# Kernel optimization log

Measured on AMD Instinct MI355X. Metric: run time of the kernel, lower is better.

The kernel has to match this reference:

```python
import jax, jax.numpy as jnp
import numpy as np

N = 50000
H = 8          # heads
C = 10         # out channels per head
F_IN = 128
NEG_SLOPE = 0.2


def _glorot(key, shape, fan_in):
    return jax.random.normal(key, shape, dtype=jnp.float32) / np.sqrt(fan_in)


def setup_inputs() -> dict:
    key = jax.random.key(0)
    ks = jax.random.split(key, 16)
    x = jax.random.normal(ks[0], (N, F_IN), dtype=jnp.float32)
    edge_index = jax.random.randint(ks[1], (2, 1600000), 0, N, dtype=jnp.int64)
    inp = {"x": x, "edge_index": edge_index}
    dims = [F_IN, H * C, H * C]  # input dim of each of the 3 layers
    k = 2
    for i, din in enumerate(dims):
        inp[f"Wl{i}"] = _glorot(ks[k + 0], (din, H * C), din)
        inp[f"Wr{i}"] = _glorot(ks[k + 1], (din, H * C), din)
        inp[f"att{i}"] = _glorot(ks[k + 2], (H, C), C)
        inp[f"b{i}"] = jnp.zeros((H * C,), dtype=jnp.float32)
        k += 3
    return inp


def gatv2_layer(x, Wl, Wr, att, b, src, dst):
    # GATv2Conv (PyG defaults): separate lin_l/lin_r, e = att . leaky_relu(xl_j + xr_i),
    # segment softmax over incoming edges, scatter-add of alpha * xl_j, concat heads + bias.
    n = x.shape[0]
    xl = (x @ Wl).reshape(n, H, C)
    xr = (x @ Wr).reshape(n, H, C)
    e = jax.nn.leaky_relu(xl[src] + xr[dst], NEG_SLOPE)      # [E, H, C]
    score = jnp.einsum('ehc,hc->eh', e, att)                 # [E, H]
    smax = jax.ops.segment_max(score, dst, num_segments=n)   # [N, H]
    ex = jnp.exp(score - smax[dst])
    denom = jax.ops.segment_sum(ex, dst, num_segments=n)
    alpha = ex / (denom[dst] + 1e-16)                        # [E, H]
    out = jax.ops.segment_sum(alpha[:, :, None] * xl[src], dst, num_segments=n)
    return out.reshape(n, H * C) + b


def reference(x, edge_index, Wl0, Wr0, att0, b0, Wl1, Wr1, att1, b1, Wl2, Wr2, att2, b2):
    n = x.shape[0]
    # add_self_loops=True (PyG default)
    loop = jnp.arange(n, dtype=edge_index.dtype)
    src = jnp.concatenate([edge_index[0], loop])
    dst = jnp.concatenate([edge_index[1], loop])
    params = [(Wl0, Wr0, att0, b0), (Wl1, Wr1, att1, b1), (Wl2, Wr2, att2, b2)]
    for Wl, Wr, att, b in params:
        x = jax.nn.elu(gatv2_layer(x, Wl, Wr, att, b, src, dst))
    return x
```

## Files before the change

### kernel.cpp

```cpp
#include <hip/hip_runtime.h>
#include <hip/hip_bf16.h>
#include <hip/hip_fp16.h>

#define N_NODES 50000
#define HEADS 8
#define CHANS 10
#define HC 80
#define PHL 80
#define F_IN 128
#define E_EDGES 1600000
#define E_TOT (E_EDGES + N_NODES)
#define NEG_SLOPE 0.2f
#define NBUCK 3125
#define NCHUNK 128
#define CHUNK ((E_TOT + NCHUNK - 1) / NCHUNK)
#define GEMM_TILES ((N_NODES + 127) / 128)
#define NSLICE 4
#define SLICE_W 12500
#define XS_STRIDE 40
#define WS_STRIDE 40

typedef _Float16 f16x8 __attribute__((ext_vector_type(8)));
typedef float f32x4 __attribute__((ext_vector_type(4)));

#if __has_builtin(__builtin_amdgcn_fdot2) && __has_builtin(__builtin_elementwise_max)
#define USE_PK 1
typedef _Float16 h2 __attribute__((ext_vector_type(2)));
#else
#define USE_PK 0
#endif

__device__ inline void load_edge(const void* ei, int is64, int e, int& src, int& dst) {
    if (e < E_EDGES) {
        if (is64) {
            src = ((const int*)ei)[2 * e];
            dst = ((const int*)ei)[2 * (E_EDGES + e)];
        } else {
            src = ((const int*)ei)[e];
            dst = ((const int*)ei)[E_EDGES + e];
        }
    } else {
        src = dst = e - E_EDGES;
    }
}

__device__ inline int load_dst(const void* ei, int is64, int e) {
    if (e < E_EDGES) {
        if (is64) return ((const int*)ei)[2 * (E_EDGES + e)];
        return ((const int*)ei)[E_EDGES + e];
    }
    return e - E_EDGES;
}

__device__ inline int detect_is64(const void* ei, int tid, int* s_flag) {
    if (tid < 64) {
        const int* p = (const int*)ei;
        bool ok = (p[2 * tid + 1] == 0) && (p[2 * (tid + 64) + 1] == 0);
        unsigned long long m = __ballot(ok);
        if (tid == 0) *s_flag = (m == ~0ull) ? 1 : 0;
    }
    return 0;
}

__global__ void wconv_kernel(const float* __restrict__ Wl0, const float* __restrict__ Wr0,
                             const float* __restrict__ Wl1, const float* __restrict__ Wr1,
                             const float* __restrict__ Wl2, const float* __restrict__ Wr2,
                             __half* __restrict__ wt) {
    int g = blockIdx.x;
    int layer = g / 160, c = g - layer * 160;
    int kp = threadIdx.x;
    const float* Wl = (layer == 0) ? Wl0 : (layer == 1) ? Wl1 : Wl2;
    const float* Wr = (layer == 0) ? Wr0 : (layer == 1) ? Wr1 : Wr2;
    const float* W = (c < 80) ? Wl : Wr;
    int cc = (c < 80) ? c : c - 80;
    int din = (layer == 0) ? F_IN : HC;
    float v = (kp < din) ? W[kp * 80 + cc] : 0.f;
    wt[(size_t)g * 128 + kp] = __float2half_rn(v);
}

__device__ __forceinline__ void gemm_tile_body(
        int tile, const void* __restrict__ xin, int in_fp16, int nkt,
        const __half* __restrict__ wt,
        __half* __restrict__ xlh, float* __restrict__ xr,
        __half* xs, __half* ws) {
    int tid = threadIdx.x;
    int n0 = tile * 128;
    int w = tid >> 6, lane = tid & 63;
    int quad = lane >> 4, r = lane & 15;

    f32x4 acc[2][10];
    #pragma unroll
    for (int nt = 0; nt < 2; nt++)
        #pragma unroll
        for (int t = 0; t < 10; t++) acc[nt][t] = (f32x4){0.f, 0.f, 0.f, 0.f};

    int snode = tid >> 1;
    int sk = (tid & 1) * 16;
    int sg = n0 + snode;

    for (int kt = 0; kt < nkt; kt++) {
        f16x8 xv0 = (f16x8){0, 0, 0, 0, 0, 0, 0, 0}, xv1 = xv0;
        if (sg < N_NODES) {
            if (in_fp16) {
                int g0 = kt * 32 + sk;
                const uint4* p = (const uint4*)((const __half*)xin + (size_t)sg * PHL + g0);
                if (g0 < PHL)     xv0 = __builtin_bit_cast(f16x8, p[0]);
                if (g0 + 8 < PHL) xv1 = __builtin_bit_cast(f16x8, p[1]);
            } else {
                const float4* p = (const float4*)((const float*)xin + (size_t)sg * F_IN + kt * 32 + sk);
                float4 f0 = p[0], f1 = p[1], f2 = p[2], f3 = p[3];
                xv0[0] = (_Float16)f0.x; xv0[1] = (_Float16)f0.y;
                xv0[2] = (_Float16)f0.z; xv0[3] = (_Float16)f0.w;
                xv0[4] = (_Float16)f1.x; xv0[5] = (_Float16)f1.y;
                xv0[6] = (_Float16)f1.z; xv0[7] = (_Float16)f1.w;
                xv1[0] = (_Float16)f2.x; xv1[1] = (_Float16)f2.y;
                xv1[2] = (_Float16)f2.z; xv1[3] = (_Float16)f2.w;
                xv1[4] = (_Float16)f3.x; xv1[5] = (_Float16)f3.y;
                xv1[6] = (_Float16)f3.z; xv1[7] = (_Float16)f3.w;
            }
        }
        __syncthreads();
        *(uint4*)(&xs[snode * XS_STRIDE + sk]) = __builtin_bit_cast(uint4, xv0);
        *(uint4*)(&xs[snode * XS_STRIDE + sk + 8]) = __builtin_bit_cast(uint4, xv1);
        for (int u = tid; u < 640; u += 256) {
            int c = u >> 2, k8 = (u & 3) * 8;
            uint4 wv = *(const uint4*)(wt + c * 128 + kt * 32 + k8);
            *(uint4*)(&ws[c * WS_STRIDE + k8]) = wv;
        }
        __syncthreads();
        #pragma unroll
        for (int nt = 0; nt < 2; nt++) {
            f16x8 a = __builtin_bit_cast(f16x8,
                         *(const uint4*)(&xs[(w * 32 + nt * 16 + r) * XS_STRIDE + quad * 8]));
            #pragma unroll
            for (int ct = 0; ct < 10; ct++) {
                f16x8 bf = __builtin_bit_cast(f16x8,
                              *(const uint4*)(&ws[(ct * 16 + r) * WS_STRIDE + quad * 8]));
                acc[nt][ct] = __builtin_amdgcn_mfma_f32_16x16x32_f16(a, bf, acc[nt][ct], 0, 0, 0);
            }
        }
    }
    __syncthreads();
    #pragma unroll
    for (int nt = 0; nt < 2; nt++) {
        #pragma unroll
        for (int ct = 0; ct < 10; ct++) {
            int col = ct * 16 + r;
            #pragma unroll
            for (int reg = 0; reg < 4; reg++) {
                int node = n0 + w * 32 + nt * 16 + quad * 4 + reg;
                if (node < N_NODES) {
                    float v = acc[nt][ct][reg];
                    if (col < 80) xlh[(size_t)node * PHL + col] = __float2half_rn(v);
                    else          xr[(size_t)node * HC + (col - 80)] = v;
                }
            }
        }
    }
}

__global__ __launch_bounds__(256) void hist_gemm0_kernel(
        const void* ei, int* __restrict__ hist, int* __restrict__ bcount,
        const float* __restrict__ x_in, const __half* __restrict__ wt0,
        __half* __restrict__ xlh, float* __restrict__ xr) {
    __shared__ __align__(16) char smem[23056];
    __shared__ int s_is64;
    int blk = blockIdx.x;
    int tid = threadIdx.x;
    if (blk >= NCHUNK) {
        __half* xs = (__half*)smem;
        __half* ws = (__half*)(smem + 10240);
        gemm_tile_body(blk - NCHUNK, x_in, 0, 4, wt0, xlh, xr, xs, ws);
        return;
    }
    int* h = (int*)smem;
    for (int i = tid; i < NBUCK; i += 256) h[i] = 0;
    detect_is64(ei, tid, &s_is64);
    __syncthreads();
    int is64 = s_is64;
    int e0 = blk * CHUNK, e1 = min(e0 + CHUNK, E_TOT);
    for (int e = e0 + tid; e < e1; e += 4 * 256) {
        int d[4]; int cnt = 0;
        #pragma unroll
        for (int u = 0; u < 4; u++) {
            int ee = e + u * 256;
            if (ee < e1) { d[u] = load_dst(ei, is64, ee); cnt = u + 1; }
        }
        #pragma unroll
        for (int u = 0; u < 4; u++)
            if (u < cnt) atomicAdd(&h[d[u] >> 4], 1);
    }
    __syncthreads();
    for (int i = tid; i < NBUCK; i += 256) {
        int v = h[i];
        int old = v ? atomicAdd(&bcount[i], v) : 0;
        hist[(size_t)blk * NBUCK + i] = old;
    }
}

__global__ void scan_total_kernel(const int* __restrict__ total, int* __restrict__ bbase) {
    __shared__ int wsum[16];
    __shared__ int wpre[16];
    __shared__ int carry;
    int tid = threadIdx.x;
    int lane = tid & 63, w = tid >> 6;
    if (tid == 0) carry = 0;
    __syncthreads();
    for (int base = 0; base < NBUCK; base += 1024) {
        int idx = base + tid;
        int v = (idx < NBUCK) ? total[idx] : 0;
        int sv = v;
        #pragma unroll
        for (int off = 1; off < 64; off <<= 1) {
            int t = __shfl_up(sv, off, 64);
            if (lane >= off) sv += t;
        }
        if (lane == 63) wsum[w] = sv;
        __syncthreads();
        if (w == 0) {
            int s = (lane < 16) ? wsum[lane] : 0;
            #pragma unroll
            for (int off = 1; off < 16; off <<= 1) {
                int t = __shfl_up(s, off, 64);
                if (lane >= off) s += t;
            }
            if (lane < 16) wpre[lane] = s;
        }
        __syncthreads();
        int pre = carry + ((w > 0) ? wpre[w - 1] : 0);
        if (idx < NBUCK) bbase[idx] = pre + sv - v;
        __syncthreads();
        if (tid == 0) carry += wpre[15];
        __syncthreads();
    }
}

__global__ __launch_bounds__(256) void scatter_sort_kernel(
        const void* ei, const int* __restrict__ hist, const int* __restrict__ bbase,
        int* __restrict__ tmp) {
    __shared__ int cur[NBUCK];
    __shared__ int s_is64;
    int tid = threadIdx.x;
    int blk = blockIdx.x;
    for (int i = tid; i < NBUCK; i += 256)
        cur[i] = bbase[i] + hist[(size_t)blk * NBUCK + i];
    detect_is64(ei, tid, &s_is64);
    __syncthreads();
    int is64 = s_is64;
    int e0 = blk * CHUNK, e1 = min(e0 + CHUNK, E_TOT);
    for (int e = e0 + tid; e < e1; e += 4 * 256) {
        int s[4], d[4]; int cnt = 0;
        #pragma unroll
        for (int u = 0; u < 4; u++) {
            int ee = e + u * 256;
            if (ee < e1) { load_edge(ei, is64, ee, s[u], d[u]); cnt = u + 1; }
        }
        #pragma unroll
        for (int u = 0; u < 4; u++) {
            if (u < cnt) {
                int pos = atomicAdd(&cur[d[u] >> 4], 1);
                tmp[pos] = (s[u] << 4) | (d[u] & 15);
            }
        }
    }
}

__global__ __launch_bounds__(256) void node_sort_kernel(
        const int* __restrict__ tmp, const int* __restrict__ bbase,
        const int* __restrict__ total,
        int* __restrict__ adj, int* __restrict__ nstart4, int* __restrict__ deg) {
    __shared__ int h64[64];
    __shared__ int st64[64];
    __shared__ int cur64[64];
    int tid = threadIdx.x;
    int b = blockIdx.x;
    int base = bbase[b];
    int n = total[b];
    if (tid < 64) h64[tid] = 0;
    __syncthreads();
    for (int k = tid; k < n; k += 256) {
        int p = tmp[base + k];
        int src = p >> 4;
        int s = src / SLICE_W; if (s > 3) s = 3;
        atomicAdd(&h64[(p & 15) * NSLICE + s], 1);
    }
    __syncthreads();
    if (tid == 0) {
        int run = 0;
        #pragma unroll
        for (int c = 0; c < 64; c++) { st64[c] = run; cur64[c] = run; run += h64[c]; }
    }
    __syncthreads();
    for (int k = tid; k < n; k += 256) {
        int p = tmp[base + k];
        int src = p >> 4;
        int s = src / SLICE_W; if (s > 3) s = 3;
        int pos = atomicAdd(&cur64[(p & 15) * NSLICE + s], 1);
        adj[base + pos] = src;
    }
    __syncthreads();
    if (tid < 64)
        nstart4[(size_t)(b * 16 + (tid >> 2)) * NSLICE + (tid & 3)] = base + st64[tid];
    if (tid < 16) {
        int end = (tid < 15) ? st64[(tid + 1) * NSLICE] : n;
        deg[b * 16 + tid] = end - st64[tid * NSLICE];
    }
}

__global__ __launch_bounds__(256) void deghist_kernel(
        const int* __restrict__ deg, int* __restrict__ dh) {
    __shared__ int h[256];
    h[threadIdx.x] = 0;
    __syncthreads();
    int i = blockIdx.x * 256 + threadIdx.x;
    if (i < N_NODES) atomicAdd(&h[min(deg[i], 255)], 1);
    __syncthreads();
    if (h[threadIdx.x]) atomicAdd(&dh[threadIdx.x], h[threadIdx.x]);
}

__global__ __launch_bounds__(256) void degscatter_kernel(
        const int* __restrict__ deg, const int* __restrict__ dh,
        int* __restrict__ resv, int* __restrict__ perm) {
    __shared__ int sbase[256];
    __shared__ int s[256];
    __shared__ int h[256];
    __shared__ int res[256];
    __shared__ int lc[256];
    int tid = threadIdx.x;
    int idx = 255 - tid;
    int own = dh[idx];
    s[tid] = own;
    h[tid] = 0; lc[tid] = 0;
    __syncthreads();
    for (int off = 1; off < 256; off <<= 1) {
        int t = (tid >= off) ? s[tid - off] : 0;
        __syncthreads();
        s[tid] += t;
        __syncthreads();
    }
    sbase[idx] = s[tid] - own;
    __syncthreads();
    int i = blockIdx.x * 256 + tid;
    int d = (i < N_NODES) ? min(deg[i], 255) : -1;
    if (d >= 0) atomicAdd(&h[d], 1);
    __syncthreads();
    res[tid] = h[tid] ? atomicAdd(&resv[tid], h[tid]) : 0;
    __syncthreads();
    if (d >= 0) {
        int off = atomicAdd(&lc[d], 1);
        perm[sbase[d] + res[d] + off] = i;
    }
}

__global__ __launch_bounds__(256) void gemm_mfma_kernel(
        const void* __restrict__ xin, int in_fp16, int nkt,
        const __half* __restrict__ wt,
        __half* __restrict__ xlh, float* __restrict__ xr) {
    __shared__ __half xs[128 * XS_STRIDE];
    __shared__ __half ws[160 * WS_STRIDE];
    gemm_tile_body(blockIdx.x, xin, in_fp16, nkt, wt, xlh, xr, xs, ws);
}

__global__ __launch_bounds__(256, 4) void agg_kernel(
        const __half* __restrict__ xlh, const float* __restrict__ xr,
        const float* __restrict__ att, const float* __restrict__ bias,
        const int* __restrict__ nstart4, const int* __restrict__ deg,
        const int* __restrict__ adj, const int* __restrict__ perm,
        __half* __restrict__ ybuf, float* __restrict__ yout) {
    int tid = threadIdx.x;
    int b = blockIdx.x;
    int h = tid & 7;
    int split = (tid >> 3) & 1;
    int i_local = tid >> 4;
    int node = perm[b * 16 + i_local];

    int starts[5];
    #pragma unroll
    for (int s = 0; s < 4; s++) starts[s] = nstart4[(size_t)node * NSLICE + s];
    starts[4] = starts[0] + deg[node];

#if USE_PK
    h2 xrh[5], atth[5];
    #pragma unroll
    for (int p = 0; p < 5; p++) {
        xrh[p] = (h2){(_Float16)xr[(size_t)node * HC + h * CHANS + 2 * p],
                      (_Float16)xr[(size_t)node * HC + h * CHANS + 2 * p + 1]};
        atth[p] = (h2){(_Float16)att[h * CHANS + 2 * p],
                       (_Float16)att[h * CHANS + 2 * p + 1]};
    }
    const h2 k02 = {(_Float16)NEG_SLOPE, (_Float16)NEG_SLOPE};
    auto score_pk = [&](const unsigned int* wv) {
        float s = 0.f;
        #pragma unroll
        for (int p = 0; p < 5; p++) {
            h2 v = __builtin_bit_cast(h2, wv[p]);
            h2 t = v + xrh[p];
            h2 tl = __builtin_elementwise_max(t, t * k02);
            s = __builtin_amdgcn_fdot2(tl, atth[p], s, false);
        }
        return s;
    };

    float m = -1e30f, l = 0.f;
    h2 acc[5];
    #pragma unroll
    for (int p = 0; p < 5; p++) acc[p] = (h2){(_Float16)0.f, (_Float16)0.f};

    #pragma unroll
    for (int s = 0; s < NSLICE; s++) {
        int s0 = starts[s];
        int len = starts[s + 1] - s0;
        int c0 = (len + 1) >> 1;
        int cnt = split ? (len - c0) : c0;
        int k0 = s0 + split * c0;
        int kk = 0;
        for (; kk + 4 <= cnt; kk += 4) {
            unsigned int w[4][5];
            #pragma unroll
            for (int r = 0; r < 4; r++) {
                int j = adj[k0 + kk + r];
                const unsigned int* p = (const unsigned int*)(xlh + (size_t)j * PHL + h * CHANS);
                #pragma unroll
                for (int q = 0; q < 5; q++) w[r][q] = p[q];
            }
            float sc[4];
            #pragma unroll
            for (int r = 0; r < 4; r++) sc[r] = score_pk(w[r]);
            float mb = m;
            #pragma unroll
            for (int r = 0; r < 4; r++) mb = fmaxf(mb, sc[r]);
            float scale = __expf(m - mb);
            float ps = 0.f;
            #pragma unroll
            for (int r = 0; r < 4; r++) { sc[r] = __expf(sc[r] - mb); ps += sc[r]; }
            l = l * scale + ps;
            _Float16 sch = (_Float16)scale;
            h2 sch2 = (h2){sch, sch};
            #pragma unroll
            for (int p = 0; p < 5; p++) acc[p] *= sch2;
            #pragma unroll
            for (int r = 0; r < 4; r++) {
                _Float16 pr = (_Float16)sc[r];
                h2 pr2 = (h2){pr, pr};
                #pragma unroll
                for (int p = 0; p < 5; p++)
                    acc[p] += pr2 * __builtin_bit_cast(h2, w[r][p]);
            }
            m = mb;
        }
        for (; kk < cnt; kk++) {
            int j = adj[k0 + kk];
            const unsigned int* p = (const unsigned int*)(xlh + (size_t)j * PHL + h * CHANS);
            unsigned int w[5] = {p[0], p[1], p[2], p[3], p[4]};
            float sv = score_pk(w);
            float mn = fmaxf(m, sv);
            float scale = __expf(m - mn);
            float pp = __expf(sv - mn);
            l = l * scale + pp;
            _Float16 sch = (_Float16)scale, prh = (_Float16)pp;
            h2 sch2 = (h2){sch, sch}, pr2 = (h2){prh, prh};
            #pragma unroll
            for (int p5 = 0; p5 < 5; p5++)
                acc[p5] = acc[p5] * sch2 + pr2 * __builtin_bit_cast(h2, w[p5]);
            m = mn;
        }
    }

    float accm[CHANS];
    float lt;
    {
        float m2 = __shfl_xor(m, 8, 64);
        float l2 = __shfl_xor(l, 8, 64);
        float mn = fmaxf(m, m2);
        float sc1 = __expf(m - mn), sc2 = __expf(m2 - mn);
        lt = l * sc1 + l2 * sc2;
        #pragma unroll
        for (int p = 0; p < 5; p++) {
            unsigned int ua = __builtin_bit_cast(unsigned int, acc[p]);
            unsigned int ub = (unsigned int)__shfl_xor((int)ua, 8, 64);
            h2 va = __builtin_bit_cast(h2, ua);
            h2 vb = __builtin_bit_cast(h2, ub);
            accm[2 * p]     = (float)va[0] * sc1 + (float)vb[0] * sc2;
            accm[2 * p + 1] = (float)va[1] * sc1 + (float)vb[1] * sc2;
        }
    }
#else
    float xr_c[CHANS], att_c[CHANS];
    #pragma unroll
    for (int c = 0; c < CHANS; c++) {
        xr_c[c]  = xr[(size_t)node * HC + h * CHANS + c];
        att_c[c] = att[h * CHANS + c];
    }
    float m = -1e30f, l = 0.f;
    float acc[CHANS];
    #pragma unroll
    for (int c = 0; c < CHANS; c++) acc[c] = 0.f;
    for (int s = 0; s < NSLICE; s++) {
        int s0 = starts[s];
        int len = starts[s + 1] - s0;
        int c0 = (len + 1) >> 1;
        int cnt = split ? (len - c0) : c0;
        int k0 = s0 + split * c0;
        for (int kk = 0; kk < cnt; kk++) {
            int j = adj[k0 + kk];
            const __half* p = xlh + (size_t)j * PHL + h * CHANS;
            float v[CHANS];
            #pragma unroll
            for (int c = 0; c < CHANS; c++) v[c] = __half2float(p[c]);
            float sv = 0.f;
            #pragma unroll
            for (int c = 0; c < CHANS; c++) {
                float t = v[c] + xr_c[c];
                t = (t > 0.f) ? t : NEG_SLOPE * t;
                sv += att_c[c] * t;
            }
            float mn = fmaxf(m, sv);
            float scale = __expf(m - mn);
            float pp = __expf(sv - mn);
            l = l * scale + pp;
            #pragma unroll
            for (int c = 0; c < CHANS; c++) acc[c] = acc[c] * scale + pp * v[c];
            m = mn;
        }
    }
    float accm[CHANS];
    float lt;
    {
        float m2 = __shfl_xor(m, 8, 64);
        float l2 = __shfl_xor(l, 8, 64);
        float mn = fmaxf(m, m2);
        float sc1 = __expf(m - mn), sc2 = __expf(m2 - mn);
        lt = l * sc1 + l2 * sc2;
        #pragma unroll
        for (int c = 0; c < CHANS; c++) {
            float a2 = __shfl_xor(acc[c], 8, 64);
            accm[c] = acc[c] * sc1 + a2 * sc2;
        }
    }
#endif

    if (split == 0) {
        float inv = 1.f / (lt + 1e-16f);
        float z[CHANS];
        #pragma unroll
        for (int c = 0; c < CHANS; c++) {
            float t = accm[c] * inv + bias[h * CHANS + c];
            z[c] = (t > 0.f) ? t : (__expf(t) - 1.f);
        }
        if (yout) {
            #pragma unroll
            for (int c = 0; c < CHANS; c++)
                yout[(size_t)node * HC + h * CHANS + c] = z[c];
        } else {
            unsigned int* dst = (unsigned int*)(ybuf + (size_t)node * PHL + h * CHANS);
            #pragma unroll
            for (int p = 0; p < 5; p++) {
                __half2 hp = __halves2half2(__float2half_rn(z[2 * p]),
                                            __float2half_rn(z[2 * p + 1]));
                dst[p] = *(unsigned int*)&hp;
            }
        }
    }
}

extern "C" void kernel_launch(void* const* d_in, const int* in_sizes, int n_in,
                              void* d_out, int out_size, void* d_ws, size_t ws_size,
                              hipStream_t stream) {
    const float* x_in = (const float*)d_in[0];
    const void*  ei   = d_in[1];
    const float* Wl[3] = {(const float*)d_in[2], (const float*)d_in[6],  (const float*)d_in[10]};
    const float* Wr[3] = {(const float*)d_in[3], (const float*)d_in[7],  (const float*)d_in[11]};
    const float* At[3] = {(const float*)d_in[4], (const float*)d_in[8],  (const float*)d_in[12]};
    const float* Bi[3] = {(const float*)d_in[5], (const float*)d_in[9],  (const float*)d_in[13]};
    float* out = (float*)d_out;

    char* ws = (char*)d_ws;
    size_t off = 0;
    auto alloc = [&](size_t bytes) {
        void* p = ws + off;
        off += (bytes + 255) & ~(size_t)255;
        return p;
    };
    __half* xlh    = (__half*)alloc((size_t)N_NODES * PHL * sizeof(__half));
    float*  xr     = (float*)alloc((size_t)N_NODES * HC * sizeof(float));
    __half* buf16  = (__half*)alloc((size_t)N_NODES * PHL * sizeof(__half));
    __half* wt     = (__half*)alloc((size_t)3 * 160 * 128 * sizeof(__half));
    int*   tmp     = (int*)alloc((size_t)E_TOT * sizeof(int));
    int*   adj     = (int*)alloc((size_t)E_TOT * sizeof(int));
    int*   hist    = (int*)alloc((size_t)NCHUNK * NBUCK * sizeof(int));
    int*   bcount  = (int*)alloc((size_t)NBUCK * sizeof(int));
    int*   dh      = (int*)alloc(256 * sizeof(int));
    int*   resv    = (int*)alloc(256 * sizeof(int));
    int*   bbase   = (int*)alloc((size_t)NBUCK * sizeof(int));
    int*   nstart4 = (int*)alloc((size_t)N_NODES * NSLICE * sizeof(int));
    int*   deg     = (int*)alloc((size_t)N_NODES * sizeof(int));
    int*   perm    = (int*)alloc((size_t)N_NODES * sizeof(int));

    hipMemsetAsync(bcount, 0, (size_t)((char*)resv - (char*)bcount) + 1024, stream);
    wconv_kernel<<<480, 128, 0, stream>>>(Wl[0], Wr[0], Wl[1], Wr[1], Wl[2], Wr[2], wt);
    hist_gemm0_kernel<<<NCHUNK + GEMM_TILES, 256, 0, stream>>>(
        ei, hist, bcount, x_in, wt, xlh, xr);
    scan_total_kernel<<<1, 1024, 0, stream>>>(bcount, bbase);
    scatter_sort_kernel<<<NCHUNK, 256, 0, stream>>>(ei, hist, bbase, tmp);
    node_sort_kernel<<<NBUCK, 256, 0, stream>>>(tmp, bbase, bcount, adj, nstart4, deg);
    int nblocks = (N_NODES + 255) / 256;
    deghist_kernel<<<nblocks, 256, 0, stream>>>(deg, dh);
    degscatter_kernel<<<nblocks, 256, 0, stream>>>(deg, dh, resv, perm);

    const void* cur = (const void*)buf16;
    for (int layer = 0; layer < 3; layer++) {
        if (layer > 0) {
            gemm_mfma_kernel<<<GEMM_TILES, 256, 0, stream>>>(
                cur, 1, 3, wt + (size_t)layer * 160 * 128, xlh, xr);
        }
        __half* ybuf = (layer == 2) ? nullptr : buf16;
        float*  yout = (layer == 2) ? out : nullptr;
        agg_kernel<<<NBUCK, 256, 0, stream>>>(xlh, xr, At[layer], Bi[layer],
                                              nstart4, deg, adj, perm, ybuf, yout);
    }
}
```

Measured before the change: 371.1 us.

## Assign whole source slices per split lane and add 8-wide gather unroll

Each of the two threads per (node, head) used to take half of every one of the four source slices. Now each thread takes two whole slices: split 0 gets slices 0-1 and split 1 gets slices 2-3. An 8-edge unrolled batch is added ahead of the existing 4-edge loop so more independent gathers are in flight per online-softmax rescale. The slice reassignment can unbalance work between the two threads when slice sizes differ, and the 8-wide batch raises register pressure.

Result: slower. 391.1 us (+5.4%).

```diff
diff --git a/kernel.cpp b/kernel.cpp
--- a/kernel.cpp
+++ b/kernel.cpp
@@ -407,13 +407,45 @@
     for (int p = 0; p < 5; p++) acc[p] = (h2){(_Float16)0.f, (_Float16)0.f};
 
     #pragma unroll
-    for (int s = 0; s < NSLICE; s++) {
-        int s0 = starts[s];
-        int len = starts[s + 1] - s0;
-        int c0 = (len + 1) >> 1;
-        int cnt = split ? (len - c0) : c0;
-        int k0 = s0 + split * c0;
+    for (int ss = 0; ss < 2; ss++) {
+        int sl = split * 2 + ss;
+        int k0 = starts[sl];
+        int cnt = starts[sl + 1] - k0;
         int kk = 0;
+        for (; kk + 8 <= cnt; kk += 8) {
+            unsigned int w[8][5];
+            #pragma unroll
+            for (int r = 0; r < 8; r++) {
+                int j = adj[k0 + kk + r];
+                const unsigned int* p = (const unsigned int*)(xlh + (size_t)j * PHL + h * CHANS);
+                #pragma unroll
+                for (int q = 0; q < 5; q++) w[r][q] = p[q];
+            }
+            float sc[8];
+            #pragma unroll
+            for (int r = 0; r < 8; r++) sc[r] = score_pk(w[r]);
+            float mb = m;
+            #pragma unroll
+            for (int r = 0; r < 8; r++) mb = fmaxf(mb, sc[r]);
+            float scale = __expf(m - mb);
+            float ps = 0.f;
+            #pragma unroll
+            for (int r = 0; r < 8; r++) { sc[r] = __expf(sc[r] - mb); ps += sc[r]; }
+            l = l * scale + ps;
+            _Float16 sch = (_Float16)scale;
+            h2 sch2 = (h2){sch, sch};
+            #pragma unroll
+            for (int p = 0; p < 5; p++) acc[p] *= sch2;
+            #pragma unroll
+            for (int r = 0; r < 8; r++) {
+                _Float16 pr = (_Float16)sc[r];
+                h2 pr2 = (h2){pr, pr};
+                #pragma unroll
+                for (int p = 0; p < 5; p++)
+                    acc[p] += pr2 * __builtin_bit_cast(h2, w[r][p]);
+            }
+            m = mb;
+        }
         for (; kk + 4 <= cnt; kk += 4) {
             unsigned int w[4][5];
             #pragma unroll
@@ -495,12 +527,10 @@
     float acc[CHANS];
     #pragma unroll
     for (int c = 0; c < CHANS; c++) acc[c] = 0.f;
-    for (int s = 0; s < NSLICE; s++) {
-        int s0 = starts[s];
-        int len = starts[s + 1] - s0;
-        int c0 = (len + 1) >> 1;
-        int cnt = split ? (len - c0) : c0;
-        int k0 = s0 + split * c0;
+    for (int ss = 0; ss < 2; ss++) {
+        int sl = split * 2 + ss;
+        int k0 = starts[sl];
+        int cnt = starts[sl + 1] - k0;
         for (int kk = 0; kk < cnt; kk++) {
             int j = adj[k0 + kk];
             const __half* p = xlh + (size_t)j * PHL + h * CHANS;
```
